# Kernel optimization log

Hardware: AMD Instinct MI355X
Metric: run time of the kernel (lower is better)

## Reference

```python
import jax, jax.numpy as jnp
import numpy as np

B, N, D, H = 128, 32768, 768, 16
DH = D // H          # per-head hidden_size = memory_dim // num_heads = 48
BETA = 0.25          # scaling (inverse temperature)
STEPS = 5            # update_steps_max
TOPK = 4


def _ln(x, g, b):
    # torch nn.LayerNorm over last dim (biased variance, eps=1e-5), affine
    m = jnp.mean(x, axis=-1, keepdims=True)
    v = jnp.var(x, axis=-1, keepdims=True)
    return (x - m) * jax.lax.rsqrt(v + 1e-5) * g + b


def _l2norm(x):
    # F.normalize(x, dim=-1): x / max(||x||, 1e-12)
    n = jnp.linalg.norm(x, axis=-1, keepdims=True)
    return x / jnp.maximum(n, 1e-12)


def setup_inputs() -> dict:
    key = jax.random.key(0)
    ks = jax.random.split(key, 8)
    s = 0.05  # weight init scale to keep activations sane
    return {
        "query_embedding": jax.random.normal(ks[0], (B, D), jnp.float32),
        "memory_bank": jax.random.normal(ks[1], (N, D), jnp.float32),
        "ln_k_g": jnp.ones((D,), jnp.float32), "ln_k_b": jnp.zeros((D,), jnp.float32),
        "ln_q_g": jnp.ones((D,), jnp.float32), "ln_q_b": jnp.zeros((D,), jnp.float32),
        "ln_v_g": jnp.ones((D,), jnp.float32), "ln_v_b": jnp.zeros((D,), jnp.float32),
        "Wq": jax.random.normal(ks[2], (D, D), jnp.float32) * s, "bq": jnp.zeros((D,), jnp.float32),
        "Wk": jax.random.normal(ks[3], (D, D), jnp.float32) * s, "bk": jnp.zeros((D,), jnp.float32),
        "Wv": jax.random.normal(ks[4], (D, D), jnp.float32) * s, "bv": jnp.zeros((D,), jnp.float32),
        "Wo": jax.random.normal(ks[5], (D, D), jnp.float32) * s, "bo": jnp.zeros((D,), jnp.float32),
        "W1": jax.random.normal(ks[6], (D, D), jnp.float32) * s, "b1": jnp.zeros((D,), jnp.float32),
        "W2": jax.random.normal(ks[7], (D, D), jnp.float32) * s, "b2": jnp.zeros((D,), jnp.float32),
    }


def reference(query_embedding, memory_bank, ln_k_g, ln_k_b, ln_q_g, ln_q_b,
              ln_v_g, ln_v_b, Wq, bq, Wk, bk, Wv, bv, Wo, bo, W1, b1, W2, b2):
    # Affine LayerNorms on stored pattern, state pattern, pattern projection.
    # memory_bank is shared across the batch, so normalize/project it ONCE
    # instead of materializing the (B, N, D) expand from the torch code.
    stored = _ln(memory_bank, ln_k_g, ln_k_b)        # (N, D)
    state = _ln(query_embedding, ln_q_g, ln_q_b)     # (B, D) -- state pattern, seq len 1
    projp = _ln(memory_bank, ln_v_g, ln_v_b)         # (N, D)

    k = (stored @ Wk.T + bk).reshape(N, H, DH)       # (N, H, dh)
    v = (projp @ Wv.T + bv).reshape(N, H, DH)        # (N, H, dh)
    q = (state @ Wq.T + bq).reshape(B, H, DH)        # (B, H, dh)

    # Hopfield convergence: xi <- softmax(beta * xi K^T) K, repeated STEPS times
    def step(xi, _):
        attn = jax.nn.softmax(BETA * jnp.einsum('bhd,nhd->bhn', xi, k), axis=-1)
        return jnp.einsum('bhn,nhd->bhd', attn, k), None

    xi, _ = jax.lax.scan(step, q, None, length=STEPS)

    # Final readout against the (separately normalized) pattern projection V
    attn = jax.nn.softmax(BETA * jnp.einsum('bhd,nhd->bhn', xi, k), axis=-1)  # (B, H, N)
    converged = jnp.einsum('bhn,nhd->bhd', attn, v).reshape(B, D) @ Wo.T + bo  # (B, D)

    # Retrieval head: residual + MLP + cosine-sim logits + top-k
    combined = query_embedding + converged
    rq = jax.nn.relu(combined @ W1.T + b1) @ W2.T + b2
    logits = (_l2norm(rq) @ _l2norm(memory_bank).T) * 20.0   # (B, N)
    top_indices = jax.lax.top_k(logits, TOPK)[1]              # (B, TOPK)
    return top_indices, logits
```

## Files before the change

kernel.cpp:

```cpp
#include <hip/hip_runtime.h>
#include <math.h>

#define NTOT 32768
#define DMODEL 768
#define BSZ 128
#define NHEAD 16
#define DH 48
#define BETA 0.25f

typedef _Float16 f16;
typedef f16 f16x8 __attribute__((ext_vector_type(8)));
typedef f16 f16x4 __attribute__((ext_vector_type(4)));
typedef float f32x4 __attribute__((ext_vector_type(4)));

__global__ __launch_bounds__(256)
void row_stats(const float* __restrict__ X, int M, float* __restrict__ mean,
               float* __restrict__ rstd, float* __restrict__ l2inv) {
  const int row = blockIdx.x * 4 + (threadIdx.x >> 6);
  const int lane = threadIdx.x & 63;
  if (row >= M) return;
  const float* x = X + (size_t)row * DMODEL;
  float s = 0.f, s2 = 0.f;
  for (int i = lane; i < DMODEL; i += 64) {
    float v = x[i];
    s += v; s2 += v * v;
  }
#pragma unroll
  for (int off = 32; off; off >>= 1) {
    s  += __shfl_xor(s, off);
    s2 += __shfl_xor(s2, off);
  }
  if (lane == 0) {
    float mu = s * (1.f / DMODEL);
    float var = s2 * (1.f / DMODEL) - mu * mu;
    mean[row] = mu;
    rstd[row] = rsqrtf(var + 1e-5f);
    if (l2inv) l2inv[row] = 1.f / fmaxf(sqrtf(s2), 1e-12f);
  }
}

__global__ __launch_bounds__(256)
void prep_w(const float* __restrict__ Wk, const float* __restrict__ bk,
            const float* __restrict__ gk, const float* __restrict__ blnk,
            const float* __restrict__ Wv, const float* __restrict__ bv,
            const float* __restrict__ gv, const float* __restrict__ blnv,
            f16* __restrict__ Wc_hi, f16* __restrict__ Wc_lo,
            float* __restrict__ biasc) {
  const int o = blockIdx.x * 4 + (threadIdx.x >> 6);
  const int lane = threadIdx.x & 63;
  const bool isK = o < DMODEL;
  const float* W = isK ? (Wk + (size_t)o * DMODEL)
                       : (Wv + (size_t)(o - DMODEL) * DMODEL);
  const float* g   = isK ? gk : gv;
  const float* bln = isK ? blnk : blnv;
  float bacc = 0.f;
  for (int d = lane * 4; d < DMODEL; d += 256) {
    const float4 wv = *(const float4*)(W + d);
    const float4 g4 = *(const float4*)(g + d);
    const float4 b4 = *(const float4*)(bln + d);
    bacc += wv.x * b4.x + wv.y * b4.y + wv.z * b4.z + wv.w * b4.w;
    const float sv[4] = {wv.x * g4.x * 16.f, wv.y * g4.y * 16.f,
                         wv.z * g4.z * 16.f, wv.w * g4.w * 16.f};
    f16x4 h4, l4;
#pragma unroll
    for (int j = 0; j < 4; j++) {
      const f16 h = (f16)sv[j];
      h4[j] = h;
      l4[j] = (f16)(sv[j] - (float)h);
    }
    *(f16x4*)(Wc_hi + (size_t)o * DMODEL + d) = h4;
    *(f16x4*)(Wc_lo + (size_t)o * DMODEL + d) = l4;
  }
#pragma unroll
  for (int off = 32; off; off >>= 1) bacc += __shfl_xor(bacc, off);
  if (lane == 0) biasc[o] = (isK ? bk[o] : bv[o - DMODEL]) + bacc;
}

__global__ __launch_bounds__(256)
void proj_dual_mfma(const float* __restrict__ mb, const float* __restrict__ mean,
                    const float* __restrict__ rstd,
                    const f16* __restrict__ Wc_hi, const f16* __restrict__ Wc_lo,
                    const float* __restrict__ biasc,
                    f16* __restrict__ k_hi, f16* __restrict__ k_lo,
                    f16* __restrict__ v_hi, f16* __restrict__ v_lo) {
  __shared__ __align__(16) f16 As[2][128][40];
  __shared__ __align__(16) f16 Bs[2][128][40];
  const int t = threadIdx.x;
  const int n0 = blockIdx.x * 128;
  const int m0 = blockIdx.y * 128;
  const int w = t >> 6, lane = t & 63;
  const int l15 = lane & 15, lq = lane >> 4;
  const int wm = w >> 1, wn = w & 1;
  const int sr = t >> 1, sh = t & 1;
  const float mu = mean[m0 + sr];
  const float rs = rstd[m0 + sr];

  f32x4 acc[4][4];
#pragma unroll
  for (int a = 0; a < 4; a++)
#pragma unroll
    for (int b = 0; b < 4; b++)
#pragma unroll
      for (int r = 0; r < 4; r++) acc[a][b][r] = 0.f;

  for (int k0 = 0; k0 < DMODEL; k0 += 32) {
    __syncthreads();
    {
      const float* ap = mb + (size_t)(m0 + sr) * DMODEL + k0 + sh * 16;
      float x[16];
#pragma unroll
      for (int c = 0; c < 4; c++) {
        const float4 v4 = *(const float4*)(ap + c * 4);
        x[c * 4 + 0] = v4.x; x[c * 4 + 1] = v4.y;
        x[c * 4 + 2] = v4.z; x[c * 4 + 3] = v4.w;
      }
      f16x8 h0, h1, l0, l1;
#pragma unroll
      for (int j = 0; j < 8; j++) {
        const float s = (x[j] - mu) * rs;
        const f16 h = (f16)s;
        h0[j] = h; l0[j] = (f16)(s - (float)h);
      }
#pragma unroll
      for (int j = 0; j < 8; j++) {
        const float s = (x[8 + j] - mu) * rs;
        const f16 h = (f16)s;
        h1[j] = h; l1[j] = (f16)(s - (float)h);
      }
      *(f16x8*)&As[0][sr][sh * 16] = h0;
      *(f16x8*)&As[0][sr][sh * 16 + 8] = h1;
      *(f16x8*)&As[1][sr][sh * 16] = l0;
      *(f16x8*)&As[1][sr][sh * 16 + 8] = l1;
    }
    {
      const size_t boff = (size_t)(n0 + sr) * DMODEL + k0 + sh * 16;
      f16x8 bh0 = *(const f16x8*)(Wc_hi + boff);
      f16x8 bh1 = *(const f16x8*)(Wc_hi + boff + 8);
      f16x8 bl0 = *(const f16x8*)(Wc_lo + boff);
      f16x8 bl1 = *(const f16x8*)(Wc_lo + boff + 8);
      *(f16x8*)&Bs[0][sr][sh * 16] = bh0;
      *(f16x8*)&Bs[0][sr][sh * 16 + 8] = bh1;
      *(f16x8*)&Bs[1][sr][sh * 16] = bl0;
      *(f16x8*)&Bs[1][sr][sh * 16 + 8] = bl1;
    }
    __syncthreads();
    f16x8 nhh[4], nhl[4];
#pragma unroll
    for (int fm = 0; fm < 4; fm++) {
      const int row = wm * 64 + fm * 16 + l15;
      nhh[fm] = *(const f16x8*)&As[0][row][lq * 8];
      nhl[fm] = *(const f16x8*)&As[1][row][lq * 8];
    }
    f16x8 wh[4], wl[4];
#pragma unroll
    for (int fo = 0; fo < 4; fo++) {
      const int row = wn * 64 + fo * 16 + l15;
      wh[fo] = *(const f16x8*)&Bs[0][row][lq * 8];
      wl[fo] = *(const f16x8*)&Bs[1][row][lq * 8];
    }
#pragma unroll
    for (int fo = 0; fo < 4; fo++)
#pragma unroll
      for (int fm = 0; fm < 4; fm++) {
        f32x4 a = acc[fo][fm];
        a = __builtin_amdgcn_mfma_f32_16x16x32_f16(wh[fo], nhh[fm], a, 0, 0, 0);
        a = __builtin_amdgcn_mfma_f32_16x16x32_f16(wh[fo], nhl[fm], a, 0, 0, 0);
        a = __builtin_amdgcn_mfma_f32_16x16x32_f16(wl[fo], nhh[fm], a, 0, 0, 0);
        acc[fo][fm] = a;
      }
  }
  const int oc = n0 + wn * 64;
  const bool isK = oc < DMODEL;
  f16* oh = isK ? k_hi : v_hi;
  f16* ol = isK ? k_lo : v_lo;
  const int obase = (isK ? oc : oc - DMODEL) + lq * 4;
#pragma unroll
  for (int fo = 0; fo < 4; fo++) {
    const float4 bb = *(const float4*)(biasc + oc + fo * 16 + lq * 4);
    const float bbv[4] = {bb.x, bb.y, bb.z, bb.w};
    const int o = obase + fo * 16;
#pragma unroll
    for (int fm = 0; fm < 4; fm++) {
      const size_t moff = (size_t)(m0 + wm * 64 + fm * 16 + l15) * DMODEL + o;
      f16x4 h4, l4;
#pragma unroll
      for (int r = 0; r < 4; r++) {
        const float v = acc[fo][fm][r] * 0.0625f + bbv[r];
        const f16 h = (f16)v;
        h4[r] = h;
        l4[r] = (f16)(v - (float)h);
      }
      *(f16x4*)(oh + moff) = h4;
      *(f16x4*)(ol + moff) = l4;
    }
  }
}

__global__ __launch_bounds__(256)
void ln_gemm_f32(const float* __restrict__ A, const float* __restrict__ mean,
                 const float* __restrict__ rstd, const float* __restrict__ g,
                 const float* __restrict__ bln, const float* __restrict__ W,
                 const float* __restrict__ bias, float* __restrict__ out) {
  __shared__ float As[16][68];
  __shared__ float Ws[16][68];
  const int t = threadIdx.x;
  const int m0 = blockIdx.y << 6, n0 = blockIdx.x << 6;
  const int tm = t >> 4, tn = t & 15;
  const int lr = t >> 2;
  const int lk = (t & 3) << 2;
  const float muL = mean[m0 + lr];
  const float rsL = rstd[m0 + lr];
  float acc[4][4] = {};
  for (int k0 = 0; k0 < DMODEL; k0 += 16) {
    float4 a4 = *(const float4*)(A + (size_t)(m0 + lr) * DMODEL + k0 + lk);
    float4 g4 = *(const float4*)(g + k0 + lk);
    float4 b4 = *(const float4*)(bln + k0 + lk);
    As[lk + 0][lr] = (a4.x - muL) * rsL * g4.x + b4.x;
    As[lk + 1][lr] = (a4.y - muL) * rsL * g4.y + b4.y;
    As[lk + 2][lr] = (a4.z - muL) * rsL * g4.z + b4.z;
    As[lk + 3][lr] = (a4.w - muL) * rsL * g4.w + b4.w;
    float4 w4 = *(const float4*)(W + (size_t)(n0 + lr) * DMODEL + k0 + lk);
    Ws[lk + 0][lr] = w4.x;
    Ws[lk + 1][lr] = w4.y;
    Ws[lk + 2][lr] = w4.z;
    Ws[lk + 3][lr] = w4.w;
    __syncthreads();
#pragma unroll
    for (int kk = 0; kk < 16; kk++) {
      const float4 av = *(const float4*)(&As[kk][tm * 4]);
      const float4 bv = *(const float4*)(&Ws[kk][tn * 4]);
      const float a[4] = {av.x, av.y, av.z, av.w};
      const float b[4] = {bv.x, bv.y, bv.z, bv.w};
#pragma unroll
      for (int i = 0; i < 4; i++)
#pragma unroll
        for (int j = 0; j < 4; j++) acc[i][j] += a[i] * b[j];
    }
    __syncthreads();
  }
  const float4 bia = *(const float4*)(bias + n0 + tn * 4);
  const float bb[4] = {bia.x, bia.y, bia.z, bia.w};
#pragma unroll
  for (int i = 0; i < 4; i++) {
    const int m = m0 + tm * 4 + i;
    float4 o4;
    o4.x = acc[i][0] + bb[0];
    o4.y = acc[i][1] + bb[1];
    o4.z = acc[i][2] + bb[2];
    o4.w = acc[i][3] + bb[3];
    *(float4*)(out + (size_t)m * DMODEL + n0 + tn * 4) = o4;
  }
}

__global__ __launch_bounds__(256)
void gemm_bias(const float* __restrict__ A, const float* __restrict__ W,
               const float* __restrict__ bias, const float* __restrict__ add,
               float* __restrict__ out, int relu) {
  __shared__ float As[16][68];
  __shared__ float Ws[16][68];
  const int t = threadIdx.x;
  const int m0 = blockIdx.y << 6, n0 = blockIdx.x << 6;
  const int tm = t >> 4, tn = t & 15;
  const int lr = t >> 2;
  const int lk = (t & 3) << 2;
  float acc[4][4] = {};
  for (int k0 = 0; k0 < DMODEL; k0 += 16) {
    float4 a4 = *(const float4*)(A + (size_t)(m0 + lr) * DMODEL + k0 + lk);
    As[lk + 0][lr] = a4.x;
    As[lk + 1][lr] = a4.y;
    As[lk + 2][lr] = a4.z;
    As[lk + 3][lr] = a4.w;
    float4 w4 = *(const float4*)(W + (size_t)(n0 + lr) * DMODEL + k0 + lk);
    Ws[lk + 0][lr] = w4.x;
    Ws[lk + 1][lr] = w4.y;
    Ws[lk + 2][lr] = w4.z;
    Ws[lk + 3][lr] = w4.w;
    __syncthreads();
#pragma unroll
    for (int kk = 0; kk < 16; kk++) {
      const float4 av = *(const float4*)(&As[kk][tm * 4]);
      const float4 bv = *(const float4*)(&Ws[kk][tn * 4]);
      const float a[4] = {av.x, av.y, av.z, av.w};
      const float b[4] = {bv.x, bv.y, bv.z, bv.w};
#pragma unroll
      for (int i = 0; i < 4; i++)
#pragma unroll
        for (int j = 0; j < 4; j++) acc[i][j] += a[i] * b[j];
    }
    __syncthreads();
  }
  const float4 bia = *(const float4*)(bias + n0 + tn * 4);
  const float bb[4] = {bia.x, bia.y, bia.z, bia.w};
#pragma unroll
  for (int i = 0; i < 4; i++) {
    const int m = m0 + tm * 4 + i;
    float v[4];
#pragma unroll
    for (int j = 0; j < 4; j++) v[j] = acc[i][j] + bb[j];
    if (add) {
      const float4 a4 = *(const float4*)(add + (size_t)m * DMODEL + n0 + tn * 4);
      v[0] += a4.x; v[1] += a4.y; v[2] += a4.z; v[3] += a4.w;
    }
    if (relu) {
#pragma unroll
      for (int j = 0; j < 4; j++) v[j] = fmaxf(v[j], 0.f);
    }
    float4 o4 = {v[0], v[1], v[2], v[3]};
    *(float4*)(out + (size_t)m * DMODEL + n0 + tn * 4) = o4;
  }
}

__global__ __launch_bounds__(256)
void logits_gemm(const float* __restrict__ A, const float* __restrict__ Bm,
                 const float* __restrict__ ainv, const float* __restrict__ binv,
                 float* __restrict__ out) {
  __shared__ float As[16][68];
  __shared__ float Ws[16][68];
  const int t = threadIdx.x;
  const int m0 = blockIdx.y << 6, n0 = blockIdx.x << 6;
  const int tm = t >> 4, tn = t & 15;
  const int lr = t >> 2;
  const int lk = (t & 3) << 2;
  float acc[4][4] = {};
  for (int k0 = 0; k0 < DMODEL; k0 += 16) {
    float4 a4 = *(const float4*)(A + (size_t)(m0 + lr) * DMODEL + k0 + lk);
    As[lk + 0][lr] = a4.x;
    As[lk + 1][lr] = a4.y;
    As[lk + 2][lr] = a4.z;
    As[lk + 3][lr] = a4.w;
    float4 w4 = *(const float4*)(Bm + (size_t)(n0 + lr) * DMODEL + k0 + lk);
    Ws[lk + 0][lr] = w4.x;
    Ws[lk + 1][lr] = w4.y;
    Ws[lk + 2][lr] = w4.z;
    Ws[lk + 3][lr] = w4.w;
    __syncthreads();
#pragma unroll
    for (int kk = 0; kk < 16; kk++) {
      const float4 av = *(const float4*)(&As[kk][tm * 4]);
      const float4 bv = *(const float4*)(&Ws[kk][tn * 4]);
      const float a[4] = {av.x, av.y, av.z, av.w};
      const float b[4] = {bv.x, bv.y, bv.z, bv.w};
#pragma unroll
      for (int i = 0; i < 4; i++)
#pragma unroll
        for (int j = 0; j < 4; j++) acc[i][j] += a[i] * b[j];
    }
    __syncthreads();
  }
  const float4 bi4 = *(const float4*)(binv + n0 + tn * 4);
  const float bi[4] = {bi4.x, bi4.y, bi4.z, bi4.w};
#pragma unroll
  for (int i = 0; i < 4; i++) {
    const int m = m0 + tm * 4 + i;
    const float sa = 20.f * ainv[m];
    float4 o4;
    o4.x = acc[i][0] * sa * bi[0];
    o4.y = acc[i][1] * sa * bi[1];
    o4.z = acc[i][2] * sa * bi[2];
    o4.w = acc[i][3] * sa * bi[3];
    *(float4*)(out + (size_t)m * NTOT + n0 + tn * 4) = o4;
  }
}

__global__ __launch_bounds__(256)
void split_xi_k(const float* __restrict__ xi, f16* __restrict__ hi,
                f16* __restrict__ lo) {
  const int i = blockIdx.x * 256 + threadIdx.x;
  float4 v = ((const float4*)xi)[i];
  float s[4] = {v.x * BETA, v.y * BETA, v.z * BETA, v.w * BETA};
  f16x4 h4, l4;
#pragma unroll
  for (int j = 0; j < 4; j++) {
    f16 h = (f16)s[j];
    h4[j] = h;
    l4[j] = (f16)(s[j] - (float)h);
  }
  ((f16x4*)hi)[i] = h4;
  ((f16x4*)lo)[i] = l4;
}

#define FCHUNK 64
#define FROWS (NTOT / FCHUNK)

__global__ __launch_bounds__(256)
void flash_round(const f16* __restrict__ k_hi, const f16* __restrict__ k_lo,
                 const f16* __restrict__ val_hi, const f16* __restrict__ val_lo,
                 const f16* __restrict__ xi_hi, const f16* __restrict__ xi_lo,
                 float* __restrict__ part_ml, float* __restrict__ part_o) {
  const int h = blockIdx.y, chunk = blockIdx.x;
  const int tid = threadIdx.x, w = tid >> 6, lane = tid & 63;
  const int l15 = lane & 15, lq = lane >> 4;
  const int b0 = w * 32;

  __shared__ __align__(16) f16 krow[2][32][56];
  __shared__ __align__(16) f16 vT[2][48][40];
  __shared__ __align__(16) f16 pHi[4][32][40];
  __shared__ __align__(16) f16 pLo[4][32][40];

  const f16x8 zf = {};
  f16x8 xqh[2][2], xql[2][2];
#pragma unroll
  for (int bt = 0; bt < 2; bt++) {
    const size_t xoff = (size_t)(b0 + bt * 16 + l15) * DMODEL + h * DH;
    xqh[bt][0] = *(const f16x8*)(xi_hi + xoff + lq * 8);
    xql[bt][0] = *(const f16x8*)(xi_lo + xoff + lq * 8);
    const size_t xo1 = xoff + 32 + (lq & 1) * 8;
    f16x8 th = *(const f16x8*)(xi_hi + xo1);
    f16x8 tl = *(const f16x8*)(xi_lo + xo1);
    xqh[bt][1] = (lq < 2) ? th : zf;
    xql[bt][1] = (lq < 2) ? tl : zf;
  }

  float m[2] = {-1e30f, -1e30f}, lsum[2] = {0.f, 0.f};
  f32x4 O[3][2];
#pragma unroll
  for (int mt = 0; mt < 3; mt++)
#pragma unroll
    for (int bt = 0; bt < 2; bt++)
#pragma unroll
      for (int j = 0; j < 4; j++) O[mt][bt][j] = 0.f;

  const int nbase = chunk * FROWS;
  for (int it = 0; it < FROWS / 32; it++) {
    const int gn0 = nbase + it * 32;
    __syncthreads();
    for (int j = tid; j < 384; j += 256) {
      const int tsel = j / 192;
      const int q = j - tsel * 192;
      const int r = q / 6;
      const int d0 = (q - r * 6) * 8;
      const size_t goff = (size_t)(gn0 + r) * DMODEL + h * DH + d0;
      const f16* kp = (tsel ? k_lo : k_hi) + goff;
      const f16* vp = (tsel ? val_lo : val_hi) + goff;
      f16x8 kv = *(const f16x8*)kp;
      f16x8 vv = *(const f16x8*)vp;
      *(f16x8*)&krow[tsel][r][d0] = kv;
#pragma unroll
      for (int jj = 0; jj < 8; jj++) vT[tsel][d0 + jj][r] = vv[jj];
    }
    __syncthreads();

    f16x8 akh[2][2], akl[2][2];
#pragma unroll
    for (int nt = 0; nt < 2; nt++) {
      const int row = nt * 16 + l15;
      akh[nt][0] = *(const f16x8*)&krow[0][row][lq * 8];
      akl[nt][0] = *(const f16x8*)&krow[1][row][lq * 8];
      f16x8 t0 = *(const f16x8*)&krow[0][row][32 + (lq & 1) * 8];
      f16x8 t1 = *(const f16x8*)&krow[1][row][32 + (lq & 1) * 8];
      akh[nt][1] = (lq < 2) ? t0 : zf;
      akl[nt][1] = (lq < 2) ? t1 : zf;
    }
    f32x4 S[2][2];
#pragma unroll
    for (int nt = 0; nt < 2; nt++)
#pragma unroll
      for (int bt = 0; bt < 2; bt++) {
        f32x4 s = {};
        s = __builtin_amdgcn_mfma_f32_16x16x32_f16(akh[nt][0], xqh[bt][0], s, 0, 0, 0);
        s = __builtin_amdgcn_mfma_f32_16x16x32_f16(akh[nt][1], xqh[bt][1], s, 0, 0, 0);
        s = __builtin_amdgcn_mfma_f32_16x16x32_f16(akh[nt][0], xql[bt][0], s, 0, 0, 0);
        s = __builtin_amdgcn_mfma_f32_16x16x32_f16(akh[nt][1], xql[bt][1], s, 0, 0, 0);
        s = __builtin_amdgcn_mfma_f32_16x16x32_f16(akl[nt][0], xqh[bt][0], s, 0, 0, 0);
        s = __builtin_amdgcn_mfma_f32_16x16x32_f16(akl[nt][1], xqh[bt][1], s, 0, 0, 0);
        S[nt][bt] = s;
      }
    float sc[2];
#pragma unroll
    for (int bt = 0; bt < 2; bt++) {
      float mx = S[0][bt][0];
#pragma unroll
      for (int r = 1; r < 4; r++) mx = fmaxf(mx, S[0][bt][r]);
#pragma unroll
      for (int r = 0; r < 4; r++) mx = fmaxf(mx, S[1][bt][r]);
      mx = fmaxf(mx, __shfl_xor(mx, 16));
      mx = fmaxf(mx, __shfl_xor(mx, 32));
      const float mnew = fmaxf(m[bt], mx);
      sc[bt] = __expf(m[bt] - mnew);
      float ps = 0.f;
#pragma unroll
      for (int nt = 0; nt < 2; nt++) {
        f16x4 ph, pl;
#pragma unroll
        for (int r = 0; r < 4; r++) {
          const float p = __expf(S[nt][bt][r] - mnew);
          ps += p;
          const f16 hh = (f16)p;
          ph[r] = hh;
          pl[r] = (f16)(p - (float)hh);
        }
        *(f16x4*)&pHi[w][bt * 16 + l15][nt * 16 + lq * 4] = ph;
        *(f16x4*)&pLo[w][bt * 16 + l15][nt * 16 + lq * 4] = pl;
      }
      ps += __shfl_xor(ps, 16);
      ps += __shfl_xor(ps, 32);
      lsum[bt] = lsum[bt] * sc[bt] + ps;
      m[bt] = mnew;
    }
    __asm__ volatile("s_waitcnt lgkmcnt(0)" ::: "memory");
    f16x8 avh[3], avl[3];
#pragma unroll
    for (int mt = 0; mt < 3; mt++) {
      avh[mt] = *(const f16x8*)&vT[0][mt * 16 + l15][lq * 8];
      avl[mt] = *(const f16x8*)&vT[1][mt * 16 + l15][lq * 8];
    }
    f16x8 pbh[2], pbl[2];
#pragma unroll
    for (int bt = 0; bt < 2; bt++) {
      pbh[bt] = *(const f16x8*)&pHi[w][bt * 16 + l15][lq * 8];
      pbl[bt] = *(const f16x8*)&pLo[w][bt * 16 + l15][lq * 8];
    }
#pragma unroll
    for (int mt = 0; mt < 3; mt++)
#pragma unroll
      for (int bt = 0; bt < 2; bt++) {
#pragma unroll
        for (int j = 0; j < 4; j++) O[mt][bt][j] *= sc[bt];
        f32x4 o = O[mt][bt];
        o = __builtin_amdgcn_mfma_f32_16x16x32_f16(avh[mt], pbh[bt], o, 0, 0, 0);
        o = __builtin_amdgcn_mfma_f32_16x16x32_f16(avh[mt], pbl[bt], o, 0, 0, 0);
        o = __builtin_amdgcn_mfma_f32_16x16x32_f16(avl[mt], pbh[bt], o, 0, 0, 0);
        O[mt][bt] = o;
      }
  }
  const int pc = h * FCHUNK + chunk;
  if (lq == 0) {
#pragma unroll
    for (int bt = 0; bt < 2; bt++) {
      float* pm = part_ml + ((size_t)pc * BSZ + b0 + bt * 16 + l15) * 2;
      pm[0] = m[bt];
      pm[1] = lsum[bt];
    }
  }
#pragma unroll
  for (int mt = 0; mt < 3; mt++)
#pragma unroll
    for (int bt = 0; bt < 2; bt++) {
      float* po = part_o + ((size_t)pc * BSZ + b0 + bt * 16 + l15) * 48 +
                  mt * 16 + lq * 4;
      *(f32x4*)po = O[mt][bt];
    }
}

__global__ __launch_bounds__(64)
void hopfield_combine(const float* __restrict__ part_ml,
                      const float* __restrict__ part_o, float* __restrict__ dst) {
  const int bh = blockIdx.x;
  const int h = bh >> 7, b = bh & 127;
  const int c = threadIdx.x;
  __shared__ float w[64];
  const float* pm = part_ml + ((size_t)(h * 64 + c) * BSZ + b) * 2;
  const float mp = pm[0];
  const float lp = pm[1];
  float M = mp;
#pragma unroll
  for (int off = 32; off; off >>= 1) M = fmaxf(M, __shfl_xor(M, off));
  const float wp = __expf(mp - M);
  w[c] = wp;
  float L = lp * wp;
#pragma unroll
  for (int off = 32; off; off >>= 1) L += __shfl_xor(L, off);
  __syncthreads();
  if (c < DH) {
    float o = 0.f;
    for (int p = 0; p < 64; p++)
      o += part_o[((size_t)(h * 64 + p) * BSZ + b) * 48 + c] * w[p];
    dst[(size_t)b * DMODEL + h * DH + c] = o / L;
  }
}

__global__ __launch_bounds__(256)
void topk_kernel(const float* __restrict__ logits, float* __restrict__ outIdx) {
  const int b = blockIdx.x;
  const int t = threadIdx.x;
  const float* row = logits + (size_t)b * NTOT;
  float v[4] = {-1e30f, -1e30f, -1e30f, -1e30f};
  int id[4] = {0x7fffffff, 0x7fffffff, 0x7fffffff, 0x7fffffff};
  for (int n = t; n < NTOT; n += 256) {
    const float x = row[n];
    if (x > v[3]) {
      v[3] = x; id[3] = n;
#pragma unroll
      for (int s = 3; s > 0; s--) {
        const bool sw = (v[s] > v[s - 1]) || (v[s] == v[s - 1] && id[s] < id[s - 1]);
        if (sw) {
          float tv = v[s]; v[s] = v[s - 1]; v[s - 1] = tv;
          int ti = id[s]; id[s] = id[s - 1]; id[s - 1] = ti;
        }
      }
    }
  }
  __shared__ float sv[256][4];
  __shared__ int si[256][4];
#pragma unroll
  for (int j = 0; j < 4; j++) { sv[t][j] = v[j]; si[t][j] = id[j]; }
  for (int str = 128; str >= 1; str >>= 1) {
    __syncthreads();
    if (t < str) {
      float a[4], c[4];
      int ai[4], ci[4];
#pragma unroll
      for (int j = 0; j < 4; j++) {
        a[j] = sv[t][j]; ai[j] = si[t][j];
        c[j] = sv[t + str][j]; ci[j] = si[t + str][j];
      }
      float rv[4]; int ri[4];
      int p = 0, q = 0;
#pragma unroll
      for (int oo = 0; oo < 4; oo++) {
        const bool ta = (a[p] > c[q]) || (a[p] == c[q] && ai[p] < ci[q]);
        if (ta) { rv[oo] = a[p]; ri[oo] = ai[p]; p++; }
        else    { rv[oo] = c[q]; ri[oo] = ci[q]; q++; }
      }
#pragma unroll
      for (int j = 0; j < 4; j++) { sv[t][j] = rv[j]; si[t][j] = ri[j]; }
    }
  }
  if (t == 0) {
#pragma unroll
    for (int j = 0; j < 4; j++) outIdx[b * 4 + j] = (float)si[0][j];
  }
}

extern "C" void kernel_launch(void* const* d_in, const int* in_sizes, int n_in,
                              void* d_out, int out_size, void* d_ws, size_t ws_size,
                              hipStream_t stream) {
  const float* qe    = (const float*)d_in[0];
  const float* mb    = (const float*)d_in[1];
  const float* ln_kg = (const float*)d_in[2];
  const float* ln_kb = (const float*)d_in[3];
  const float* ln_qg = (const float*)d_in[4];
  const float* ln_qb = (const float*)d_in[5];
  const float* ln_vg = (const float*)d_in[6];
  const float* ln_vb = (const float*)d_in[7];
  const float* Wq = (const float*)d_in[8];
  const float* bq = (const float*)d_in[9];
  const float* Wk = (const float*)d_in[10];
  const float* bk = (const float*)d_in[11];
  const float* Wv = (const float*)d_in[12];
  const float* bv = (const float*)d_in[13];
  const float* Wo = (const float*)d_in[14];
  const float* bo = (const float*)d_in[15];
  const float* W1 = (const float*)d_in[16];
  const float* b1 = (const float*)d_in[17];
  const float* W2 = (const float*)d_in[18];
  const float* b2 = (const float*)d_in[19];

  float* out = (float*)d_out;
  float* logits = out + BSZ * 4;

  float* ws = (float*)d_ws;
  size_t off = 0;
  auto alloc = [&](size_t n) { float* p = ws + off; off += n; return p; };
  const size_t ND2 = (size_t)NTOT * DMODEL / 2;
  float* mb_mean = alloc(NTOT);
  float* mb_rstd = alloc(NTOT);
  float* mb_l2i  = alloc(NTOT);
  float* q_mean  = alloc(128);
  float* q_rstd  = alloc(128);
  float* rq_inv  = alloc(128);
  float* pad_    = alloc(384);
  f16* k_hi = (f16*)alloc(ND2);
  f16* k_lo = (f16*)alloc(ND2);
  f16* v_hi = (f16*)alloc(ND2);
  f16* v_lo = (f16*)alloc(ND2);
  float* part_ml = alloc((size_t)NHEAD * FCHUNK * BSZ * 2);
  float* part_o  = alloc((size_t)NHEAD * FCHUNK * BSZ * 48);
  float* xi   = alloc((size_t)BSZ * DMODEL);
  float* conv = alloc((size_t)BSZ * DMODEL);
  float* comb = alloc((size_t)BSZ * DMODEL);
  float* h1   = alloc((size_t)BSZ * DMODEL);
  f16* xi_hi = (f16*)alloc((size_t)BSZ * DMODEL / 2);
  f16* xi_lo = (f16*)alloc((size_t)BSZ * DMODEL / 2);
  f16* Wc_hi = (f16*)alloc((size_t)2 * DMODEL * DMODEL / 2);
  f16* Wc_lo = (f16*)alloc((size_t)2 * DMODEL * DMODEL / 2);
  float* biasc = alloc(2 * DMODEL);
  (void)ws_size; (void)in_sizes; (void)n_in; (void)out_size; (void)pad_;

  row_stats<<<NTOT / 4, 256, 0, stream>>>(mb, NTOT, mb_mean, mb_rstd, mb_l2i);
  row_stats<<<BSZ / 4, 256, 0, stream>>>(qe, BSZ, q_mean, q_rstd, nullptr);
  prep_w<<<2 * DMODEL / 4, 256, 0, stream>>>(Wk, bk, ln_kg, ln_kb,
                                             Wv, bv, ln_vg, ln_vb,
                                             Wc_hi, Wc_lo, biasc);

  proj_dual_mfma<<<dim3(2 * DMODEL / 128, NTOT / 128), 256, 0, stream>>>(
      mb, mb_mean, mb_rstd, Wc_hi, Wc_lo, biasc, k_hi, k_lo, v_hi, v_lo);
  ln_gemm_f32<<<dim3(DMODEL / 64, BSZ / 64), 256, 0, stream>>>(
      qe, q_mean, q_rstd, ln_qg, ln_qb, Wq, bq, xi);

  for (int r = 0; r < 6; r++) {
    const f16* valHi = (r == 5) ? v_hi : k_hi;
    const f16* valLo = (r == 5) ? v_lo : k_lo;
    float* dst = (r == 5) ? conv : xi;
    split_xi_k<<<96, 256, 0, stream>>>(xi, xi_hi, xi_lo);
    flash_round<<<dim3(FCHUNK, NHEAD), 256, 0, stream>>>(
        k_hi, k_lo, valHi, valLo, xi_hi, xi_lo, part_ml, part_o);
    hopfield_combine<<<BSZ * NHEAD, 64, 0, stream>>>(part_ml, part_o, dst);
  }

  gemm_bias<<<dim3(DMODEL / 64, BSZ / 64), 256, 0, stream>>>(conv, Wo, bo, qe, comb, 0);
  gemm_bias<<<dim3(DMODEL / 64, BSZ / 64), 256, 0, stream>>>(comb, W1, b1, nullptr, h1, 1);
  float* rq = conv;
  gemm_bias<<<dim3(DMODEL / 64, BSZ / 64), 256, 0, stream>>>(h1, W2, b2, nullptr, rq, 0);

  row_stats<<<BSZ / 4, 256, 0, stream>>>(rq, BSZ, q_mean, q_rstd, rq_inv);
  logits_gemm<<<dim3(NTOT / 64, BSZ / 64), 256, 0, stream>>>(rq, mb, rq_inv, mb_l2i, logits);

  topk_kernel<<<BSZ, 256, 0, stream>>>(logits, out);
}
```

Before: 1.465 ms.

## Pre-split normalized memory bank to fp16 and stage GEMM tiles via direct global-to-LDS loads

Adds a separate pass that LayerNorm-normalizes the memory bank and writes hi/lo fp16 halves to global memory. The projection GEMM can then load both operands straight into LDS with global_load_lds, using an XOR-swizzled layout, instead of converting fp32 in registers on every tile. The conversion is no longer repeated across the 12 column blocks, and register-staged LDS writes go away. In exchange it adds an extra kernel plus a 2x N x D fp16 buffer write and read-back.

```diff
diff --git a/kernel.cpp b/kernel.cpp
--- a/kernel.cpp
+++ b/kernel.cpp
@@ -36,6 +36,33 @@
     mean[row] = mu;
     rstd[row] = rsqrtf(var + 1e-5f);
     if (l2inv) l2inv[row] = 1.f / fmaxf(sqrtf(s2), 1e-12f);
+  }
+}
+
+__global__ __launch_bounds__(256)
+void norm_split_mb(const float* __restrict__ mb, const float* __restrict__ mean,
+                   const float* __restrict__ rstd, f16* __restrict__ nh_hi,
+                   f16* __restrict__ nh_lo) {
+  const int row = blockIdx.x * 4 + (threadIdx.x >> 6);
+  const int lane = threadIdx.x & 63;
+  const float mu = mean[row];
+  const float rs = rstd[row];
+  const float* x = mb + (size_t)row * DMODEL;
+  f16* oh = nh_hi + (size_t)row * DMODEL;
+  f16* ol = nh_lo + (size_t)row * DMODEL;
+  for (int d = lane * 4; d < DMODEL; d += 256) {
+    const float4 v = *(const float4*)(x + d);
+    const float s[4] = {(v.x - mu) * rs, (v.y - mu) * rs,
+                        (v.z - mu) * rs, (v.w - mu) * rs};
+    f16x4 h4, l4;
+#pragma unroll
+    for (int j = 0; j < 4; j++) {
+      const f16 h = (f16)s[j];
+      h4[j] = h;
+      l4[j] = (f16)(s[j] - (float)h);
+    }
+    *(f16x4*)(oh + d) = h4;
+    *(f16x4*)(ol + d) = l4;
   }
 }
 
@@ -77,23 +104,21 @@
 }
 
 __global__ __launch_bounds__(256)
-void proj_dual_mfma(const float* __restrict__ mb, const float* __restrict__ mean,
-                    const float* __restrict__ rstd,
+void proj_dual_mfma(const f16* __restrict__ nh_hi, const f16* __restrict__ nh_lo,
                     const f16* __restrict__ Wc_hi, const f16* __restrict__ Wc_lo,
                     const float* __restrict__ biasc,
                     f16* __restrict__ k_hi, f16* __restrict__ k_lo,
                     f16* __restrict__ v_hi, f16* __restrict__ v_lo) {
-  __shared__ __align__(16) f16 As[2][128][40];
-  __shared__ __align__(16) f16 Bs[2][128][40];
+  __shared__ __align__(16) f16 As[128][64];
+  __shared__ __align__(16) f16 Bs[128][64];
   const int t = threadIdx.x;
   const int n0 = blockIdx.x * 128;
   const int m0 = blockIdx.y * 128;
   const int w = t >> 6, lane = t & 63;
   const int l15 = lane & 15, lq = lane >> 4;
   const int wm = w >> 1, wn = w & 1;
-  const int sr = t >> 1, sh = t & 1;
-  const float mu = mean[m0 + sr];
-  const float rs = rstd[m0 + sr];
+  const int sc = (lane & 7) ^ (lane >> 3);
+  const int srow = lane >> 3;
 
   f32x4 acc[4][4];
 #pragma unroll
@@ -105,58 +130,37 @@
 
   for (int k0 = 0; k0 < DMODEL; k0 += 32) {
     __syncthreads();
-    {
-      const float* ap = mb + (size_t)(m0 + sr) * DMODEL + k0 + sh * 16;
-      float x[16];
-#pragma unroll
-      for (int c = 0; c < 4; c++) {
-        const float4 v4 = *(const float4*)(ap + c * 4);
-        x[c * 4 + 0] = v4.x; x[c * 4 + 1] = v4.y;
-        x[c * 4 + 2] = v4.z; x[c * 4 + 3] = v4.w;
-      }
-      f16x8 h0, h1, l0, l1;
-#pragma unroll
-      for (int j = 0; j < 8; j++) {
-        const float s = (x[j] - mu) * rs;
-        const f16 h = (f16)s;
-        h0[j] = h; l0[j] = (f16)(s - (float)h);
-      }
-#pragma unroll
-      for (int j = 0; j < 8; j++) {
-        const float s = (x[8 + j] - mu) * rs;
-        const f16 h = (f16)s;
-        h1[j] = h; l1[j] = (f16)(s - (float)h);
-      }
-      *(f16x8*)&As[0][sr][sh * 16] = h0;
-      *(f16x8*)&As[0][sr][sh * 16 + 8] = h1;
-      *(f16x8*)&As[1][sr][sh * 16] = l0;
-      *(f16x8*)&As[1][sr][sh * 16 + 8] = l1;
-    }
-    {
-      const size_t boff = (size_t)(n0 + sr) * DMODEL + k0 + sh * 16;
-      f16x8 bh0 = *(const f16x8*)(Wc_hi + boff);
-      f16x8 bh1 = *(const f16x8*)(Wc_hi + boff + 8);
-      f16x8 bl0 = *(const f16x8*)(Wc_lo + boff);
-      f16x8 bl1 = *(const f16x8*)(Wc_lo + boff + 8);
-      *(f16x8*)&Bs[0][sr][sh * 16] = bh0;
-      *(f16x8*)&Bs[0][sr][sh * 16 + 8] = bh1;
-      *(f16x8*)&Bs[1][sr][sh * 16] = bl0;
-      *(f16x8*)&Bs[1][sr][sh * 16 + 8] = bl1;
-    }
-    __syncthreads();
+#pragma unroll
+    for (int i = 0; i < 4; i++) {
+      const int rb = (w * 4 + i) * 8;
+      const f16* asrc = ((sc < 4) ? nh_hi : nh_lo) +
+          (size_t)(m0 + rb + srow) * DMODEL + k0 + (sc & 3) * 8;
+      __builtin_amdgcn_global_load_lds(
+          (__attribute__((address_space(1))) void*)asrc,
+          (__attribute__((address_space(3))) void*)&As[rb][0], 16, 0, 0);
+      const f16* bsrc = ((sc < 4) ? Wc_hi : Wc_lo) +
+          (size_t)(n0 + rb + srow) * DMODEL + k0 + (sc & 3) * 8;
+      __builtin_amdgcn_global_load_lds(
+          (__attribute__((address_space(1))) void*)bsrc,
+          (__attribute__((address_space(3))) void*)&Bs[rb][0], 16, 0, 0);
+    }
+    __syncthreads();
+
     f16x8 nhh[4], nhl[4];
 #pragma unroll
     for (int fm = 0; fm < 4; fm++) {
       const int row = wm * 64 + fm * 16 + l15;
-      nhh[fm] = *(const f16x8*)&As[0][row][lq * 8];
-      nhl[fm] = *(const f16x8*)&As[1][row][lq * 8];
+      const int e = row & 7;
+      nhh[fm] = *(const f16x8*)&As[row][(lq ^ e) * 8];
+      nhl[fm] = *(const f16x8*)&As[row][((lq + 4) ^ e) * 8];
     }
     f16x8 wh[4], wl[4];
 #pragma unroll
     for (int fo = 0; fo < 4; fo++) {
       const int row = wn * 64 + fo * 16 + l15;
-      wh[fo] = *(const f16x8*)&Bs[0][row][lq * 8];
-      wl[fo] = *(const f16x8*)&Bs[1][row][lq * 8];
+      const int e = row & 7;
+      wh[fo] = *(const f16x8*)&Bs[row][(lq ^ e) * 8];
+      wl[fo] = *(const f16x8*)&Bs[row][((lq + 4) ^ e) * 8];
     }
 #pragma unroll
     for (int fo = 0; fo < 4; fo++)
@@ -664,6 +668,8 @@
   f16* k_lo = (f16*)alloc(ND2);
   f16* v_hi = (f16*)alloc(ND2);
   f16* v_lo = (f16*)alloc(ND2);
+  f16* nh_hi = (f16*)alloc(ND2);
+  f16* nh_lo = (f16*)alloc(ND2);
   float* part_ml = alloc((size_t)NHEAD * FCHUNK * BSZ * 2);
   float* part_o  = alloc((size_t)NHEAD * FCHUNK * BSZ * 48);
   float* xi   = alloc((size_t)BSZ * DMODEL);
@@ -679,12 +685,13 @@
 
   row_stats<<<NTOT / 4, 256, 0, stream>>>(mb, NTOT, mb_mean, mb_rstd, mb_l2i);
   row_stats<<<BSZ / 4, 256, 0, stream>>>(qe, BSZ, q_mean, q_rstd, nullptr);
+  norm_split_mb<<<NTOT / 4, 256, 0, stream>>>(mb, mb_mean, mb_rstd, nh_hi, nh_lo);
   prep_w<<<2 * DMODEL / 4, 256, 0, stream>>>(Wk, bk, ln_kg, ln_kb,
                                              Wv, bv, ln_vg, ln_vb,
                                              Wc_hi, Wc_lo, biasc);
 
   proj_dual_mfma<<<dim3(2 * DMODEL / 128, NTOT / 128), 256, 0, stream>>>(
-      mb, mb_mean, mb_rstd, Wc_hi, Wc_lo, biasc, k_hi, k_lo, v_hi, v_lo);
+      nh_hi, nh_lo, Wc_hi, Wc_lo, biasc, k_hi, k_lo, v_hi, v_lo);
   ln_gemm_f32<<<dim3(DMODEL / 64, BSZ / 64), 256, 0, stream>>>(
       qe, q_mean, q_rstd, ln_qg, ln_qb, Wq, bq, xi);
 
```

After: 1.489 ms. Within noise of the previous version (+1.6%).
